# Kernel tuning notes

Measured on AMD Instinct MI355X. Metric: run time of the kernel, lower is better.

The kernel has to match this reference:

```python
import jax, jax.numpy as jnp
import numpy as np

N_START, N_TO, E, H = 100000, 50000, 1000000, 128

def setup_inputs() -> dict:
    key = jax.random.key(0)
    ks = jax.random.split(key, 8)
    return {
        "z_start": jax.random.normal(ks[0], (N_START, H), dtype=jnp.float32),
        "z_to": jax.random.normal(ks[1], (N_TO, H), dtype=jnp.float32),
        "row": jax.random.randint(ks[2], (E,), 0, N_START, dtype=jnp.int64),
        "col": jax.random.randint(ks[3], (E,), 0, N_TO, dtype=jnp.int64),
        "W1": jax.random.normal(ks[4], (2 * H, H), dtype=jnp.float32) * (1.0 / np.sqrt(2 * H)),
        "b1": jnp.zeros((H,), dtype=jnp.float32),
        "W2": jax.random.normal(ks[5], (H, 1), dtype=jnp.float32) * (1.0 / np.sqrt(H)),
        "b2": jnp.zeros((1,), dtype=jnp.float32),
    }

def reference(z_start, z_to, row, col, W1, b1, W2, b2):
    # gather node embeddings by edge endpoints, concat along feature dim
    z = jnp.concatenate([z_start[row], z_to[col]], axis=-1)  # [E, 2H]
    h = jax.nn.relu(z @ W1 + b1)                              # [E, H]
    out = h @ W2 + b2                                         # [E, 1]
    return out.reshape(-1)
```

## Files before the change

### kernel.cpp

```cpp
#include <hip/hip_runtime.h>
#include <hip/hip_bf16.h>
#include <stdint.h>

typedef unsigned short u16;
typedef unsigned char u8;
typedef unsigned long long u64;
typedef __attribute__((ext_vector_type(8))) short short8;
typedef __attribute__((ext_vector_type(4))) float float4v;
typedef __attribute__((ext_vector_type(2))) _Float16 v2h;

__device__ __forceinline__ u16 f2bf(float x) {
    union { float f; unsigned int u; } v; v.f = x;
    unsigned int r = v.u + 0x7fffu + ((v.u >> 16) & 1u);
    return (u16)(r >> 16);
}

__device__ __forceinline__ void ld_g2l16(const void* g, void* l) {
    __builtin_amdgcn_global_load_lds(
        (const __attribute__((address_space(1))) void*)g,
        (__attribute__((address_space(3))) void*)l, 16, 0, 0);
}

__device__ __forceinline__ v2h mk2h(unsigned int u) {
    union { unsigned int u; v2h h; } c; c.u = u; return c.h;
}

__device__ __forceinline__ float dot2acc(v2h a, v2h b, float s) {
#if __has_builtin(__builtin_amdgcn_fdot2)
    return __builtin_amdgcn_fdot2(a, b, s, false);
#else
    return fmaf((float)a[0], (float)b[0], fmaf((float)a[1], (float)b[1], s));
#endif
}

__device__ __forceinline__ unsigned perm_even(unsigned x, unsigned k64) {
#if __has_builtin(__builtin_amdgcn_perm)
    return __builtin_amdgcn_perm(x, k64, 0x00060004u);
#else
    return (x & 0x00FF00FFu) | 0x64006400u;
#endif
}
__device__ __forceinline__ unsigned perm_odd(unsigned x, unsigned k64) {
#if __has_builtin(__builtin_amdgcn_perm)
    return __builtin_amdgcn_perm(x, k64, 0x00070005u);
#else
    return ((x >> 8) & 0x00FF00FFu) | 0x64006400u;
#endif
}


__global__ __launch_bounds__(256) void w1_pack(
    const float* __restrict__ W1, u16* __restrict__ w1p, int* __restrict__ cursor)
{
    if (blockIdx.x == 0 && threadIdx.x < 8) cursor[threadIdx.x] = 0;
    int w = blockIdx.x * 256 + threadIdx.x;
    int lanep = w & 63, t = (w >> 6) & 7, kc = w >> 9;
    short8 o;
#pragma unroll
    for (int j = 0; j < 8; ++j) {
        int k = kc * 32 + (lanep >> 4) * 8 + j;
        int n = t * 16 + (lanep & 15);
        o[j] = (short)f2bf(W1[k * 128 + n]);
    }
    *(short8*)(w1p + (size_t)w * 8) = o;
}

__global__ __launch_bounds__(256, 3) void gemm_bin(
    const float* __restrict__ zs, const float* __restrict__ zt,
    const u16* __restrict__ w1p, const float* __restrict__ b1,
    u8* __restrict__ U8, u8* __restrict__ V8,
    float* __restrict__ su, float* __restrict__ sv,
    int M1, int M2, int nU, int nGemm,
    const int* __restrict__ row, const int* __restrict__ col,
    u64* __restrict__ tup, int* __restrict__ cursor,
    int E, float binv, int C,
    const float* __restrict__ W1, const float* __restrict__ W2,
    const float* __restrict__ b2, float* __restrict__ out)
{
    __shared__ u16 Blds[16384];
    __shared__ int lcnt[8];
    __shared__ int lbase[8];

    if ((int)blockIdx.x < nGemm) {
        const int tid = threadIdx.x, wave = tid >> 6, lane = tid & 63;
        const int m15 = lane & 15, quad = lane >> 4;
        const bool isV = (int)blockIdx.x >= nU;
        const float* zsrc = isV ? zt : zs;
        u8* dst = isV ? V8 : U8;
        float* sdst = isV ? sv : su;
        const int row0 = (isV ? ((int)blockIdx.x - nU) : (int)blockIdx.x) * 128;
        const int M = isV ? M2 : M1;
        const int nrows = (M - row0) < 128 ? (M - row0) : 128;
        const char* wsrc = (const char*)(w1p + (isV ? 16384 : 0));

        float4 afl[2][4][2];
#pragma unroll
        for (int mtl = 0; mtl < 2; ++mtl) {
            int r = wave * 32 + mtl * 16 + m15;
            int rr = r < nrows ? r : (nrows - 1);
            const float* rowp = zsrc + (size_t)(row0 + rr) * 128 + quad * 8;
#pragma unroll
            for (int kc = 0; kc < 4; ++kc) {
                afl[mtl][kc][0] = *(const float4*)(rowp + kc * 32);
                afl[mtl][kc][1] = *(const float4*)(rowp + kc * 32 + 4);
            }
        }

#pragma unroll
        for (int it = 0; it < 8; ++it) {
            int off = (wave * 8 + it) * 1024;
            ld_g2l16(wsrc + off + lane * 16, (char*)Blds + off);
        }

        __builtin_amdgcn_s_waitcnt(0);
        __syncthreads();

        short8 Af[2][4];
#pragma unroll
        for (int mtl = 0; mtl < 2; ++mtl)
#pragma unroll
            for (int kc = 0; kc < 4; ++kc) {
                float4 x = afl[mtl][kc][0], y = afl[mtl][kc][1];
                short8 o;
                o[0] = (short)f2bf(x.x); o[1] = (short)f2bf(x.y);
                o[2] = (short)f2bf(x.z); o[3] = (short)f2bf(x.w);
                o[4] = (short)f2bf(y.x); o[5] = (short)f2bf(y.y);
                o[6] = (short)f2bf(y.z); o[7] = (short)f2bf(y.w);
                Af[mtl][kc] = o;
            }

        float4v acc[2][8];
#pragma unroll
        for (int a = 0; a < 2; ++a)
#pragma unroll
            for (int b = 0; b < 8; ++b)
                acc[a][b] = (float4v){0.f, 0.f, 0.f, 0.f};

#pragma unroll
        for (int kc = 0; kc < 4; ++kc) {
#pragma unroll
            for (int t = 0; t < 8; ++t) {
                short8 Bf = *(const short8*)((const char*)Blds + (kc * 8 + t) * 1024 + lane * 16);
#pragma unroll
                for (int mtl = 0; mtl < 2; ++mtl)
                    acc[mtl][t] = __builtin_amdgcn_mfma_f32_16x16x32_bf16(
                        Af[mtl][kc], Bf, acc[mtl][t], 0, 0, 0);
            }
        }

        float b1v[8];
#pragma unroll
        for (int t = 0; t < 8; ++t) b1v[t] = isV ? 0.f : b1[t * 16 + m15];

#pragma unroll
        for (int mtl = 0; mtl < 2; ++mtl) {
#pragma unroll
            for (int ri = 0; ri < 4; ++ri) {
                const int rr = wave * 32 + mtl * 16 + quad * 4 + ri;
                float vals[8];
                float vmax = 0.f;
#pragma unroll
                for (int t = 0; t < 8; ++t) {
                    float x = acc[mtl][t][ri] + b1v[t];
                    vals[t] = x;
                    vmax = fmaxf(vmax, fabsf(x));
                }
                vmax = fmaxf(vmax, __shfl_xor(vmax, 1));
                vmax = fmaxf(vmax, __shfl_xor(vmax, 2));
                vmax = fmaxf(vmax, __shfl_xor(vmax, 4));
                vmax = fmaxf(vmax, __shfl_xor(vmax, 8));
                const float scl = vmax * (1.f / 127.f);
                const float rs = vmax > 0.f ? 127.f / vmax : 0.f;
                if (rr < nrows) {
                    if (m15 == 0) sdst[row0 + rr] = scl;
                    unsigned wlo = 0, whi = 0;
#pragma unroll
                    for (int t = 0; t < 4; ++t) {
                        int q = __float2int_rn(vals[t] * rs);
                        q = q > 127 ? 127 : (q < -127 ? -127 : q);
                        wlo |= (unsigned)(q + 128) << (8 * t);
                    }
#pragma unroll
                    for (int t = 4; t < 8; ++t) {
                        int q = __float2int_rn(vals[t] * rs);
                        q = q > 127 ? 127 : (q < -127 ? -127 : q);
                        whi |= (unsigned)(q + 128) << (8 * (t - 4));
                    }
                    uint2 pk; pk.x = wlo; pk.y = whi;
                    *(uint2*)(dst + (size_t)(row0 + rr) * 128 + m15 * 8) = pk;
                }
            }
        }
    } else {
        const int tid = threadIdx.x;
        if (tid < 8) lcnt[tid] = 0;
        __syncthreads();
        const int eb = ((int)blockIdx.x - nGemm) * 4096;
        int rr[16], cc[16], bb[16], rk[16];
#pragma unroll
        for (int it = 0; it < 16; ++it) {
            int e = eb + it * 256 + tid;
            rk[it] = -1;
            if (e < E) {
                int r = row[e], c = col[e];
                int b = (int)((float)r * binv);
                b = b > 7 ? 7 : b;
                rr[it] = r; cc[it] = c; bb[it] = b;
                rk[it] = atomicAdd(&lcnt[b], 1);
            }
        }
        __syncthreads();
        if (tid < 8) lbase[tid] = atomicAdd(&cursor[tid], lcnt[tid]);
        __syncthreads();
#pragma unroll
        for (int it = 0; it < 16; ++it) {
            if (rk[it] < 0) continue;
            int e = eb + it * 256 + tid;
            int slot = lbase[bb[it]] + rk[it];
            if (slot < C) {
                tup[(size_t)bb[it] * C + slot] =
                    (u64)(unsigned)rr[it] | ((u64)(unsigned)cc[it] << 17) | ((u64)(unsigned)e << 34);
            } else {
                const float* za = zs + (size_t)rr[it] * 128;
                const float* zb = zt + (size_t)cc[it] * 128;
                float s = 0.f;
                for (int j = 0; j < 128; ++j) {
                    float h = b1[j];
                    for (int k = 0; k < 128; ++k) h = fmaf(za[k], W1[k * 128 + j], h);
                    for (int k = 0; k < 128; ++k) h = fmaf(zb[k], W1[(128 + k) * 128 + j], h);
                    h = fmaxf(h, 0.f);
                    s = fmaf(h, W2[j], s);
                }
                out[e] = s + b2[0];
            }
        }
    }
}

__global__ __launch_bounds__(256) void edge_out(
    const u8* __restrict__ U8, const u8* __restrict__ V8,
    const float* __restrict__ su, const float* __restrict__ sv,
    const u64* __restrict__ tup, const int* __restrict__ cursor,
    const float* __restrict__ W2, const float* __restrict__ b2,
    float* __restrict__ out, int C, int chunks_per_bin)
{
    const int tid = threadIdx.x, m7 = tid & 7, g = tid >> 3;
    const int bin = (int)blockIdx.x & 7;
    int chunk = (int)blockIdx.x >> 3;
    int cnt = cursor[bin];
    cnt = cnt < C ? cnt : C;
    if (chunk * 256 >= cnt) return;

    v2h w2e[4], w2o[4];
#pragma unroll
    for (int w = 0; w < 4; ++w) {
        int c0 = 2 * m7 + (w >> 1);
        int tb = (w & 1) * 4;
        w2e[w] = (v2h){(_Float16)W2[(tb + 0) * 16 + c0], (_Float16)W2[(tb + 2) * 16 + c0]};
        w2o[w] = (v2h){(_Float16)W2[(tb + 1) * 16 + c0], (_Float16)W2[(tb + 3) * 16 + c0]};
    }
    const float b2v = b2[0];
    const v2h zero2 = (v2h){(_Float16)0.f, (_Float16)0.f};
    const _Float16 mh = (_Float16)(-1152.f);
    const v2h m1152 = (v2h){mh, mh};
    const unsigned k64 = 0x64646464u;
    const u64* tb8 = tup + (size_t)bin * C;

    u64 t[8];
#pragma unroll
    for (int it = 0; it < 8; ++it) {
        int idx = chunk * 256 + it * 32 + g;
        t[it] = tb8[idx < cnt ? idx : cnt - 1];
    }

    for (; chunk * 256 < cnt; chunk += chunks_per_bin) {
        const int base = chunk * 256;
        __builtin_amdgcn_sched_barrier(0);

        uint4 qu[8], qv[8];
        float fsu[8], fsv[8];
#pragma unroll
        for (int it = 0; it < 8; ++it) {
            int r = (int)(t[it] & 0x1FFFF);
            int c = (int)((t[it] >> 17) & 0x1FFFF);
            qu[it] = *(const uint4*)(U8 + (size_t)(unsigned)r * 128 + m7 * 16);
            qv[it] = *(const uint4*)(V8 + (size_t)(unsigned)c * 128 + m7 * 16);
            fsu[it] = su[r];
            fsv[it] = sv[c];
        }
        __builtin_amdgcn_sched_barrier(0);

        const int nbase = (chunk + chunks_per_bin) * 256;
        u64 tn[8];
        const bool more = nbase < cnt;
        if (more) {
#pragma unroll
            for (int it = 0; it < 8; ++it) {
                int idx = nbase + it * 32 + g;
                tn[it] = tb8[idx < cnt ? idx : cnt - 1];
            }
        }
        __builtin_amdgcn_sched_barrier(0);

#pragma unroll
        for (int it = 0; it < 8; ++it) {
            const float a = fsu[it], b = fsv[it];
            const _Float16 ah = (_Float16)a, bh = (_Float16)b;
            const v2h a2 = (v2h){ah, ah}, bb2 = (v2h){bh, bh};
            const unsigned int* uw = (const unsigned int*)&qu[it];
            const unsigned int* vw = (const unsigned int*)&qv[it];
            float s = 0.f;
#pragma unroll
            for (int w = 0; w < 4; ++w) {
                v2h due = mk2h(perm_even(uw[w], k64)) + m1152;
                v2h duo = mk2h(perm_odd (uw[w], k64)) + m1152;
                v2h dve = mk2h(perm_even(vw[w], k64)) + m1152;
                v2h dvo = mk2h(perm_odd (vw[w], k64)) + m1152;
                v2h he = __builtin_elementwise_fma(a2, due, bb2 * dve);
                he = __builtin_elementwise_max(he, zero2);
                s = dot2acc(he, w2e[w], s);
                v2h ho = __builtin_elementwise_fma(a2, duo, bb2 * dvo);
                ho = __builtin_elementwise_max(ho, zero2);
                s = dot2acc(ho, w2o[w], s);
            }
            s += __shfl_xor(s, 1);
            s += __shfl_xor(s, 2);
            s += __shfl_xor(s, 4);
            int idx = base + it * 32 + g;
            if (m7 == 0 && idx < cnt) out[(int)(t[it] >> 34)] = s + b2v;
        }
        if (more) {
#pragma unroll
            for (int it = 0; it < 8; ++it) t[it] = tn[it];
        }
    }
}

__global__ __launch_bounds__(256) void edge_mlp_naive(
    const float* __restrict__ zs, const float* __restrict__ zt,
    const int* __restrict__ row, const int* __restrict__ col,
    const float* __restrict__ W1, const float* __restrict__ b1,
    const float* __restrict__ W2, const float* __restrict__ b2,
    float* __restrict__ out, int E)
{
    __shared__ float zr[4][256];
    int wave = threadIdx.x >> 6, lane = threadIdx.x & 63;
    int e = blockIdx.x * 4 + wave;
    int ec = e < E ? e : E - 1;
    const float* a = zs + (size_t)row[ec] * 128;
    const float* bb = zt + (size_t)col[ec] * 128;
    zr[wave][lane] = a[lane];
    zr[wave][64 + lane] = a[64 + lane];
    zr[wave][128 + lane] = bb[lane];
    zr[wave][192 + lane] = bb[64 + lane];
    __syncthreads();
    float h0 = b1[lane], h1 = b1[64 + lane];
    for (int k = 0; k < 256; ++k) {
        float zk = zr[wave][k];
        h0 = fmaf(zk, W1[k * 128 + lane], h0);
        h1 = fmaf(zk, W1[k * 128 + 64 + lane], h1);
    }
    h0 = h0 > 0.f ? h0 : 0.f;
    h1 = h1 > 0.f ? h1 : 0.f;
    float s = fmaf(h0, W2[lane], h1 * W2[64 + lane]);
    for (int m = 1; m < 64; m <<= 1) s += __shfl_xor(s, m);
    if (lane == 0 && e < E) out[e] = s + b2[0];
}

extern "C" void kernel_launch(void* const* d_in, const int* in_sizes, int n_in,
                              void* d_out, int out_size, void* d_ws, size_t ws_size,
                              hipStream_t stream) {
    const float* zs = (const float*)d_in[0];
    const float* zt = (const float*)d_in[1];
    const int*  row = (const int*)d_in[2];
    const int*  col = (const int*)d_in[3];
    const float* W1 = (const float*)d_in[4];
    const float* b1 = (const float*)d_in[5];
    const float* W2 = (const float*)d_in[6];
    const float* b2 = (const float*)d_in[7];
    float* out = (float*)d_out;

    const int nzs = in_sizes[0];
    const int nzt = in_sizes[1];
    const int E   = in_sizes[2];
    const int M1  = nzs / 128;
    const int M2  = nzt / 128;

    int C = 65536;
    while (C < E / 4 + 1024) C <<= 1;

    const size_t tup_b = (size_t)8 * C * 8;
    const size_t need = tup_b + 64 + (size_t)M1 * 4 + (size_t)M2 * 4 + 65536
                      + (size_t)nzs + (size_t)nzt;
    const bool shapes_ok = (M1 <= 131072) && (M2 <= 131072) && (E > 0) && (E < (1 << 30));

    if (!shapes_ok || ws_size < need) {
        int nb = (E + 3) / 4;
        edge_mlp_naive<<<nb, 256, 0, stream>>>(zs, zt, row, col, W1, b1, W2, b2, out, E);
        return;
    }

    u64* tup    = (u64*)d_ws;
    int* cursor = (int*)((char*)d_ws + tup_b);
    float* su   = (float*)((char*)cursor + 64);
    float* sv   = su + M1;
    u16* w1p    = (u16*)(sv + M2);
    u8* U8      = (u8*)(w1p + 32768);
    u8* V8      = U8 + (size_t)nzs;

    w1_pack<<<16, 256, 0, stream>>>(W1, w1p, cursor);

    const int nU = (M1 + 127) / 128;
    const int nV = (M2 + 127) / 128;
    const int nGemm = nU + nV;
    const int nBin = (E + 4095) / 4096;
    const int rpb = (M1 + 7) / 8;
    const float binv = 1.0f / (float)rpb;

    gemm_bin<<<nGemm + nBin, 256, 0, stream>>>(
        zs, zt, w1p, b1, U8, V8, su, sv, M1, M2, nU, nGemm,
        row, col, tup, cursor, E, binv, C, W1, W2, b2, out);

    const int cpb = 512;
    edge_out<<<8 * cpb, 256, 0, stream>>>(U8, V8, su, sv, tup, cursor, W2, b2, out, C, cpb);
}
```

Before: 165.1 us.

## Process four row tiles per GEMM block with register-prefetched next tile

Each GEMM block now handles four consecutive 128-row tiles instead of one. It loads the packed W1 slice into LDS once per block, and while computing the current tile it prefetches the next tile's fp32 rows into registers. This amortizes the LDS weight load and block launch cost and overlaps global loads with MFMA work. In exchange, occupancy is lowered to 2 blocks per SM and there are 4x fewer GEMM blocks, which could underfill the GPU. Tail tiles are clamped and recomputed redundantly, which is idempotent.

Measured after the change: 172.7 us. +4.6%, slower.

```diff
diff --git a/kernel.cpp b/kernel.cpp
--- a/kernel.cpp
+++ b/kernel.cpp
@@ -65,12 +65,12 @@
     *(short8*)(w1p + (size_t)w * 8) = o;
 }
 
-__global__ __launch_bounds__(256, 3) void gemm_bin(
+__global__ __launch_bounds__(256, 2) void gemm_bin(
     const float* __restrict__ zs, const float* __restrict__ zt,
     const u16* __restrict__ w1p, const float* __restrict__ b1,
     u8* __restrict__ U8, u8* __restrict__ V8,
     float* __restrict__ su, float* __restrict__ sv,
-    int M1, int M2, int nU, int nGemm,
+    int M1, int M2, int nUB, int nGemm,
     const int* __restrict__ row, const int* __restrict__ col,
     u64* __restrict__ tup, int* __restrict__ cursor,
     int E, float binv, int C,
@@ -84,27 +84,15 @@
     if ((int)blockIdx.x < nGemm) {
         const int tid = threadIdx.x, wave = tid >> 6, lane = tid & 63;
         const int m15 = lane & 15, quad = lane >> 4;
-        const bool isV = (int)blockIdx.x >= nU;
+        const int bid = (int)blockIdx.x;
+        const bool isV = bid >= nUB;
         const float* zsrc = isV ? zt : zs;
         u8* dst = isV ? V8 : U8;
         float* sdst = isV ? sv : su;
-        const int row0 = (isV ? ((int)blockIdx.x - nU) : (int)blockIdx.x) * 128;
         const int M = isV ? M2 : M1;
-        const int nrows = (M - row0) < 128 ? (M - row0) : 128;
+        const int ntt = (M + 127) >> 7;
+        const int t0 = (isV ? bid - nUB : bid) * 4;
         const char* wsrc = (const char*)(w1p + (isV ? 16384 : 0));
-
-        float4 afl[2][4][2];
-#pragma unroll
-        for (int mtl = 0; mtl < 2; ++mtl) {
-            int r = wave * 32 + mtl * 16 + m15;
-            int rr = r < nrows ? r : (nrows - 1);
-            const float* rowp = zsrc + (size_t)(row0 + rr) * 128 + quad * 8;
-#pragma unroll
-            for (int kc = 0; kc < 4; ++kc) {
-                afl[mtl][kc][0] = *(const float4*)(rowp + kc * 32);
-                afl[mtl][kc][1] = *(const float4*)(rowp + kc * 32 + 4);
-            }
-        }
 
 #pragma unroll
         for (int it = 0; it < 8; ++it) {
@@ -112,82 +100,126 @@
             ld_g2l16(wsrc + off + lane * 16, (char*)Blds + off);
         }
 
+        float4 win[2][4][2];
+        {
+            const int tt = t0 < ntt ? t0 : ntt - 1;
+            const int row0 = tt * 128;
+            int nr = M - row0; nr = nr < 128 ? nr : 128;
+#pragma unroll
+            for (int mtl = 0; mtl < 2; ++mtl) {
+                int r_ = wave * 32 + mtl * 16 + m15;
+                int rc = r_ < nr ? r_ : nr - 1;
+                const float* rp = zsrc + (size_t)(row0 + rc) * 128 + quad * 8;
+#pragma unroll
+                for (int kc = 0; kc < 4; ++kc) {
+                    win[mtl][kc][0] = *(const float4*)(rp + kc * 32);
+                    win[mtl][kc][1] = *(const float4*)(rp + kc * 32 + 4);
+                }
+            }
+        }
+
         __builtin_amdgcn_s_waitcnt(0);
         __syncthreads();
 
-        short8 Af[2][4];
-#pragma unroll
-        for (int mtl = 0; mtl < 2; ++mtl)
+#pragma unroll
+        for (int i = 0; i < 4; ++i) {
+            const int tcur = (t0 + i) < ntt ? (t0 + i) : ntt - 1;
+            const int row0 = tcur * 128;
+            const int nrows = (M - row0) < 128 ? (M - row0) : 128;
+
+            short8 Af[2][4];
+#pragma unroll
+            for (int mtl = 0; mtl < 2; ++mtl)
+#pragma unroll
+                for (int kc = 0; kc < 4; ++kc) {
+                    float4 x = win[mtl][kc][0], y = win[mtl][kc][1];
+                    short8 o;
+                    o[0] = (short)f2bf(x.x); o[1] = (short)f2bf(x.y);
+                    o[2] = (short)f2bf(x.z); o[3] = (short)f2bf(x.w);
+                    o[4] = (short)f2bf(y.x); o[5] = (short)f2bf(y.y);
+                    o[6] = (short)f2bf(y.z); o[7] = (short)f2bf(y.w);
+                    Af[mtl][kc] = o;
+                }
+            __builtin_amdgcn_sched_barrier(0);
+
+            if (i < 3) {
+                const int tn = (t0 + i + 1) < ntt ? (t0 + i + 1) : ntt - 1;
+                const int row0n = tn * 128;
+                int nrn = M - row0n; nrn = nrn < 128 ? nrn : 128;
+#pragma unroll
+                for (int mtl = 0; mtl < 2; ++mtl) {
+                    int r_ = wave * 32 + mtl * 16 + m15;
+                    int rc = r_ < nrn ? r_ : nrn - 1;
+                    const float* rp = zsrc + (size_t)(row0n + rc) * 128 + quad * 8;
+#pragma unroll
+                    for (int kc = 0; kc < 4; ++kc) {
+                        win[mtl][kc][0] = *(const float4*)(rp + kc * 32);
+                        win[mtl][kc][1] = *(const float4*)(rp + kc * 32 + 4);
+                    }
+                }
+            }
+            __builtin_amdgcn_sched_barrier(0);
+
+            float4v acc[2][8];
+#pragma unroll
+            for (int a = 0; a < 2; ++a)
+#pragma unroll
+                for (int b = 0; b < 8; ++b)
+                    acc[a][b] = (float4v){0.f, 0.f, 0.f, 0.f};
+
 #pragma unroll
             for (int kc = 0; kc < 4; ++kc) {
-                float4 x = afl[mtl][kc][0], y = afl[mtl][kc][1];
-                short8 o;
-                o[0] = (short)f2bf(x.x); o[1] = (short)f2bf(x.y);
-                o[2] = (short)f2bf(x.z); o[3] = (short)f2bf(x.w);
-                o[4] = (short)f2bf(y.x); o[5] = (short)f2bf(y.y);
-                o[6] = (short)f2bf(y.z); o[7] = (short)f2bf(y.w);
-                Af[mtl][kc] = o;
-            }
-
-        float4v acc[2][8];
-#pragma unroll
-        for (int a = 0; a < 2; ++a)
-#pragma unroll
-            for (int b = 0; b < 8; ++b)
-                acc[a][b] = (float4v){0.f, 0.f, 0.f, 0.f};
-
-#pragma unroll
-        for (int kc = 0; kc < 4; ++kc) {
-#pragma unroll
-            for (int t = 0; t < 8; ++t) {
-                short8 Bf = *(const short8*)((const char*)Blds + (kc * 8 + t) * 1024 + lane * 16);
-#pragma unroll
-                for (int mtl = 0; mtl < 2; ++mtl)
-                    acc[mtl][t] = __builtin_amdgcn_mfma_f32_16x16x32_bf16(
-                        Af[mtl][kc], Bf, acc[mtl][t], 0, 0, 0);
-            }
-        }
-
-        float b1v[8];
-#pragma unroll
-        for (int t = 0; t < 8; ++t) b1v[t] = isV ? 0.f : b1[t * 16 + m15];
-
-#pragma unroll
-        for (int mtl = 0; mtl < 2; ++mtl) {
-#pragma unroll
-            for (int ri = 0; ri < 4; ++ri) {
-                const int rr = wave * 32 + mtl * 16 + quad * 4 + ri;
-                float vals[8];
-                float vmax = 0.f;
 #pragma unroll
                 for (int t = 0; t < 8; ++t) {
-                    float x = acc[mtl][t][ri] + b1v[t];
-                    vals[t] = x;
-                    vmax = fmaxf(vmax, fabsf(x));
-                }
-                vmax = fmaxf(vmax, __shfl_xor(vmax, 1));
-                vmax = fmaxf(vmax, __shfl_xor(vmax, 2));
-                vmax = fmaxf(vmax, __shfl_xor(vmax, 4));
-                vmax = fmaxf(vmax, __shfl_xor(vmax, 8));
-                const float scl = vmax * (1.f / 127.f);
-                const float rs = vmax > 0.f ? 127.f / vmax : 0.f;
-                if (rr < nrows) {
-                    if (m15 == 0) sdst[row0 + rr] = scl;
-                    unsigned wlo = 0, whi = 0;
-#pragma unroll
-                    for (int t = 0; t < 4; ++t) {
-                        int q = __float2int_rn(vals[t] * rs);
-                        q = q > 127 ? 127 : (q < -127 ? -127 : q);
-                        wlo |= (unsigned)(q + 128) << (8 * t);
+                    short8 Bf = *(const short8*)((const char*)Blds + (kc * 8 + t) * 1024 + lane * 16);
+#pragma unroll
+                    for (int mtl = 0; mtl < 2; ++mtl)
+                        acc[mtl][t] = __builtin_amdgcn_mfma_f32_16x16x32_bf16(
+                            Af[mtl][kc], Bf, acc[mtl][t], 0, 0, 0);
+                }
+            }
+
+            float b1v[8];
+#pragma unroll
+            for (int t = 0; t < 8; ++t) b1v[t] = isV ? 0.f : b1[t * 16 + m15];
+
+#pragma unroll
+            for (int mtl = 0; mtl < 2; ++mtl) {
+#pragma unroll
+                for (int ri = 0; ri < 4; ++ri) {
+                    const int rr = wave * 32 + mtl * 16 + quad * 4 + ri;
+                    float vals[8];
+                    float vmax = 0.f;
+#pragma unroll
+                    for (int t = 0; t < 8; ++t) {
+                        float x = acc[mtl][t][ri] + b1v[t];
+                        vals[t] = x;
+                        vmax = fmaxf(vmax, fabsf(x));
                     }
-#pragma unroll
-                    for (int t = 4; t < 8; ++t) {
-                        int q = __float2int_rn(vals[t] * rs);
-                        q = q > 127 ? 127 : (q < -127 ? -127 : q);
-                        whi |= (unsigned)(q + 128) << (8 * (t - 4));
+                    vmax = fmaxf(vmax, __shfl_xor(vmax, 1));
+                    vmax = fmaxf(vmax, __shfl_xor(vmax, 2));
+                    vmax = fmaxf(vmax, __shfl_xor(vmax, 4));
+                    vmax = fmaxf(vmax, __shfl_xor(vmax, 8));
+                    const float scl = vmax * (1.f / 127.f);
+                    const float rs = vmax > 0.f ? 127.f / vmax : 0.f;
+                    if (rr < nrows) {
+                        if (m15 == 0) sdst[row0 + rr] = scl;
+                        unsigned wlo = 0, whi = 0;
+#pragma unroll
+                        for (int t = 0; t < 4; ++t) {
+                            int q = __float2int_rn(vals[t] * rs);
+                            q = q > 127 ? 127 : (q < -127 ? -127 : q);
+                            wlo |= (unsigned)(q + 128) << (8 * t);
+                        }
+#pragma unroll
+                        for (int t = 4; t < 8; ++t) {
+                            int q = __float2int_rn(vals[t] * rs);
+                            q = q > 127 ? 127 : (q < -127 ? -127 : q);
+                            whi |= (unsigned)(q + 128) << (8 * (t - 4));
+                        }
+                        uint2 pk; pk.x = wlo; pk.y = whi;
+                        *(uint2*)(dst + (size_t)(row0 + rr) * 128 + m15 * 8) = pk;
                     }
-                    uint2 pk; pk.x = wlo; pk.y = whi;
-                    *(uint2*)(dst + (size_t)(row0 + rr) * 128 + m15 * 8) = pk;
                 }
             }
         }
@@ -410,15 +442,17 @@
 
     w1_pack<<<16, 256, 0, stream>>>(W1, w1p, cursor);
 
-    const int nU = (M1 + 127) / 128;
-    const int nV = (M2 + 127) / 128;
-    const int nGemm = nU + nV;
+    const int nUt = (M1 + 127) / 128;
+    const int nVt = (M2 + 127) / 128;
+    const int nUB = (nUt + 3) / 4;
+    const int nVB = (nVt + 3) / 4;
+    const int nGemm = nUB + nVB;
     const int nBin = (E + 4095) / 4096;
     const int rpb = (M1 + 7) / 8;
     const float binv = 1.0f / (float)rpb;
 
     gemm_bin<<<nGemm + nBin, 256, 0, stream>>>(
-        zs, zt, w1p, b1, U8, V8, su, sv, M1, M2, nU, nGemm,
+        zs, zt, w1p, b1, U8, V8, su, sv, M1, M2, nUB, nGemm,
         row, col, tup, cursor, E, binv, C, W1, W2, b2, out);
 
     const int cpb = 512;
```
